# Kernel optimization log

Measured on AMD Instinct MI355X. Metric: run time of the kernel, lower is better.

## Reference

```python
import jax, jax.numpy as jnp
import numpy as np
import math

B, L, T, NW, D, DL = 4, 48, 16, 20, 256, 64


def setup_inputs() -> dict:
    key = jax.random.key(0)
    ks = jax.random.split(key, 16)
    n = lambda k, s, sc=1.0: jax.random.normal(k, s, dtype=jnp.float32) * sc
    z = lambda s: jnp.zeros(s, dtype=jnp.float32)
    return {
        'f_c': n(ks[0], (B, L, L, T, D), 0.5),
        'f_m': n(ks[1], (B, L, L, D), 0.5),
        'f_b': n(ks[2], (B, L, D), 0.5),
        'f_w': n(ks[3], (B, NW, D), 0.5),
        'f_s': n(ks[4], (B, D), 0.5),
        'bWq': n(ks[5], (D, D), 0.02), 'bbq': z((D,)),
        'bWk': n(ks[6], (D, D), 0.02), 'bbk': z((D,)),
        'cWq': n(ks[7], (DL, DL), 0.05), 'cbq': z((DL,)),
        'cWk': n(ks[8], (DL, DL), 0.05), 'cbk': z((DL,)),
        'dcc_w': n(ks[9], (DL, D), 0.05), 'dcc_b': z((DL,)),
        'dcw_w': n(ks[10], (DL, D), 0.05), 'dcw_b': z((DL,)),
        'dcs_w': n(ks[11], (DL, D), 0.05), 'dcs_b': z((DL,)),
        'ucc_w': n(ks[12], (D, DL), 0.05), 'ucc_b': z((D,)),
        'mfb_w': n(ks[13], (L, L), 0.05), 'mfb_b': z((L,)),
        'mfc_w': n(ks[14], (L, L), 0.05), 'mfc_b': z((L,)),
    }


def _smi_forward(f_c, f_m, f_b, f_w, f_s, bWq, bbq, bWk, bbk, cWq, cbq, cWk, cbk,
                 dcc_w, dcc_b, dcw_w, dcw_b, dcs_w, dcs_b, ucc_w, ucc_b,
                 mfb_w, mfb_b, mfc_w, mfc_b):
    lin = lambda x, W, b: x @ W.T + b  # torch Linear / 1x1 conv over channel-last

    def boundary_unit(fb, fm):
        # cross attention over words
        q = lin(fb, bWq, bbq)                                   # (B,L,D)
        k = lin(f_w, bWk, bbk)                                  # (B,Nw,D)
        aw = jax.nn.softmax(jnp.einsum('bld,bnd->bln', q, k) / math.sqrt(D), axis=-1)
        f_baq = jnp.einsum('bln,bnd->bld', aw, f_w)
        f_bq = fb * (f_baq + f_s[:, None, :])
        A_b = jax.nn.softmax(jnp.einsum('bld,bmd->blm', f_bq, f_bq) / math.sqrt(D), axis=-1)
        f_bb = jnp.einsum('blm,bmd->bld', A_b, fb)
        g_m = jax.nn.sigmoid(fm * f_s[:, None, None, :])        # (B,L,L,D)
        f_bm = jnp.einsum('blm,blmd->bld', A_b, g_m * fm)
        return f_bb + fb + f_bm

    def content_unit(fc, fm):
        f_c_hat = lin(fc, dcc_w, dcc_b)                         # (B,L,L,T,dl)
        f_w_hat = lin(f_w, dcw_w, dcw_b)                        # (B,Nw,dl)
        f_s_hat = lin(f_s, dcs_w, dcs_b)                        # (B,dl)
        q = lin(f_c_hat, cWq, cbq)
        k = lin(f_w_hat, cWk, cbk)
        aw = jax.nn.softmax(jnp.einsum('blmtd,bnd->blmtn', q, k) / math.sqrt(DL), axis=-1)
        f_caq = jnp.einsum('blmtn,bnd->blmtd', aw, f_w_hat)
        f_cq = f_c_hat * (f_caq + f_s_hat[:, None, None, None, :])
        A_c = jax.nn.softmax(jnp.einsum('blmtd,blmsd->blmts', f_cq, f_cq) / math.sqrt(DL), axis=-1)
        f_cc_hat = jnp.einsum('blmts,blmsd->blmtd', A_c, f_c_hat)
        f_cc = lin(f_cc_hat, ucc_w, ucc_b)                      # (B,L,L,T,D)
        g_m = jax.nn.sigmoid(fm * f_s[:, None, None, :])
        return f_cc + fc + (g_m * fm)[:, :, :, None, :]

    def moment_unit(fc, fm, fb):
        prod = fb[:, :, None, :] * fb[:, None, :, :]            # (B,L,L,D)
        conv_fb = jnp.einsum('oi,bimd->bomd', mfb_w, prod) + mfb_b[None, :, None, None]
        fc_mean = jnp.mean(fc, axis=3)                          # (B,L,L,D)
        conv_fc = jnp.einsum('oi,bimd->bomd', mfc_w, fc_mean) + mfc_b[None, :, None, None]
        return conv_fb + conv_fc + fm

    cu, bu, mu = f_c, f_b, f_m
    for _ in range(3):
        cu_n = content_unit(cu, mu)
        bu_n = boundary_unit(bu, mu)
        mu = moment_unit(cu_n, mu, bu_n)
        cu, bu = cu_n, bu_n
    return (mu, bu)


def reference(f_c, f_m, f_b, f_w, f_s, bWq, bbq, bWk, bbk, cWq, cbq, cWk, cbk,
              dcc_w, dcc_b, dcw_w, dcw_b, dcs_w, dcs_b, ucc_w, ucc_b,
              mfb_w, mfb_b, mfc_w, mfc_b):
    return _smi_forward(f_c, f_m, f_b, f_w, f_s, bWq, bbq, bWk, bbk, cWq, cbq, cWk, cbk,
                        dcc_w, dcc_b, dcw_w, dcw_b, dcs_w, dcs_b, ucc_w, ucc_b,
                        mfb_w, mfb_b, mfc_w, mfc_b)
```

## Files before the change

### kernel.cpp

```cpp
#include <hip/hip_runtime.h>

#define BB 4
#define LL 48
#define TT 16
#define NWW 20
#define DD 256
#define DLL 64

typedef __attribute__((ext_vector_type(8))) short s8v;
typedef __attribute__((ext_vector_type(4))) float f4v;
typedef unsigned short ushort_t;

#define OFF_CU     0ull
#define OFF_CM     75497472ull
#define OFF_BU0    84934656ull
#define OFF_BU1    85131264ull
#define OFF_FBQ    85327872ull
#define OFF_FWH    85524480ull
#define OFF_FSH    85544960ull
#define OFF_KB     85545984ull
#define OFF_BWQT   85627904ull
#define OFF_WBT    85890048ull
#define OFF_WCT    85899264ull
#define OFF_DCCF   85908480ull
#define OFF_CWQF   85941248ull
#define OFF_UCCF   85949440ull
#define OFF_KCF    85982208ull
#define OFF_FWHTF  85998592ull

static __device__ __forceinline__ ushort_t f2bf(float f){
  unsigned u = __float_as_uint(f);
  return (ushort_t)((u + 0x7FFFu + ((u>>16)&1u)) >> 16);
}
static __device__ __forceinline__ float bf2f(ushort_t h){
  return __uint_as_float(((unsigned)h)<<16);
}
static __device__ __forceinline__ void st64(void* p, float a, float b, float c, float d){
  uint2 v; v.x = (unsigned)f2bf(a) | ((unsigned)f2bf(b)<<16);
  v.y = (unsigned)f2bf(c) | ((unsigned)f2bf(d)<<16);
  *(uint2*)p = v;
}

#define ADR64(row, cb) (((row)<<7) + ((cb) ^ (((row)&7)<<4)))
#define ADR32(row, cb) (((row)<<6) + ((cb) ^ (((row)&3)<<4)))

#define MFMA(a,b,c) __builtin_amdgcn_mfma_f32_16x16x32_bf16((a),(b),(c),0,0,0)

template<int FIRST>
__global__ __launch_bounds__(256)
void content_kernel(const void* cusrc_, ushort_t* cudst, float* __restrict__ cm,
                    const float* __restrict__ fm_src, const float* __restrict__ fsg,
                    const float* __restrict__ fsh, const float* __restrict__ dccb,
                    const float* __restrict__ cbq, const float* __restrict__ uccb,
                    const ushort_t* __restrict__ dccf, const ushort_t* __restrict__ cwqf,
                    const ushort_t* __restrict__ uccf, const ushort_t* __restrict__ kcf,
                    const ushort_t* __restrict__ fwhtf)
{
  __shared__ __align__(16) char sm_all[4][8192];
  const int wid = threadIdx.x >> 6;
  const int lane = threadIdx.x & 63;
  char* sm = sm_all[wid];
  const int t = lane & 15, g = lane >> 4;
  const int tile = blockIdx.x*4 + wid;
  const int b = tile / (LL*LL);

  {
    f4v z = {0.f,0.f,0.f,0.f};
    *(f4v*)(sm + 4096 + ADR32(lane, 32)) = z;
    *(f4v*)(sm + 4096 + ADR32(lane, 48)) = z;
  }

  s8v xb[8];
  if (FIRST){
    const float* xp = (const float*)cusrc_ + (size_t)tile*4096 + t*DD + g*8;
    #pragma unroll
    for (int kk=0;kk<8;kk++){
      f4v lo = *(const f4v*)(xp + kk*32);
      f4v hi = *(const f4v*)(xp + kk*32 + 4);
      s8v v;
      v[0]=(short)f2bf(lo[0]); v[1]=(short)f2bf(lo[1]);
      v[2]=(short)f2bf(lo[2]); v[3]=(short)f2bf(lo[3]);
      v[4]=(short)f2bf(hi[0]); v[5]=(short)f2bf(hi[1]);
      v[6]=(short)f2bf(hi[2]); v[7]=(short)f2bf(hi[3]);
      xb[kk]=v;
    }
  } else {
    const ushort_t* xp = (const ushort_t*)cusrc_ + (size_t)tile*4096 + t*DD + g*8;
    #pragma unroll
    for (int kk=0;kk<8;kk++) xb[kk] = *(const s8v*)(xp + kk*32);
  }

  f4v accH[4];
  {
    f4v z = {0.f,0.f,0.f,0.f};
    accH[0]=z; accH[1]=z; accH[2]=z; accH[3]=z;
  }
  #pragma unroll
  for (int kk=0;kk<8;kk++){
    #pragma unroll
    for (int m0=0;m0<4;m0++){
      s8v a = *(const s8v*)(dccf + (((m0<<3)+kk)<<9) + (lane<<3));
      accH[m0] = MFMA(a, xb[kk], accH[m0]);
    }
  }
  #pragma unroll
  for (int m0=0;m0<4;m0++){
    f4v acc = accH[m0];
    f4v bi = *(const f4v*)(dccb + m0*16 + g*4);
    acc[0]+=bi[0]; acc[1]+=bi[1]; acc[2]+=bi[2]; acc[3]+=bi[3];
    accH[m0]=acc;
    st64(sm + ADR64(t, m0*32 + g*8), acc[0],acc[1],acc[2],acc[3]);
    #pragma unroll
    for (int r=0;r<4;r++)
      *(ushort_t*)(sm + 4096 + ADR32(m0*16 + g*4 + r, t*2)) = f2bf(acc[r]);
  }
  __syncthreads();

  s8v hb0 = *(const s8v*)(sm + ADR64(t, g*16));
  s8v hb1 = *(const s8v*)(sm + ADR64(t, 64 + g*16));
  #pragma unroll
  for (int m0=0;m0<4;m0++){
    f4v acc = {0.f,0.f,0.f,0.f};
    s8v a0 = *(const s8v*)(cwqf + (((m0<<1)  )<<9) + (lane<<3));
    s8v a1 = *(const s8v*)(cwqf + (((m0<<1)+1)<<9) + (lane<<3));
    acc = MFMA(a0, hb0, acc);
    acc = MFMA(a1, hb1, acc);
    f4v bi = *(const f4v*)(cbq + m0*16 + g*4);
    st64(sm + 2048 + ADR64(t, m0*32 + g*8),
         acc[0]+bi[0], acc[1]+bi[1], acc[2]+bi[2], acc[3]+bi[3]);
  }
  __syncthreads();

  s8v qb0 = *(const s8v*)(sm + 2048 + ADR64(t, g*16));
  s8v qb1 = *(const s8v*)(sm + 2048 + ADR64(t, 64 + g*16));
  f4v sA[2];
  #pragma unroll
  for (int m0=0;m0<2;m0++){
    f4v acc = {0.f,0.f,0.f,0.f};
    s8v a0 = *(const s8v*)(kcf + (b<<11) + (((m0<<1)  )<<9) + (lane<<3));
    s8v a1 = *(const s8v*)(kcf + (b<<11) + (((m0<<1)+1)<<9) + (lane<<3));
    acc = MFMA(a0, qb0, acc);
    acc = MFMA(a1, qb1, acc);
    sA[m0]=acc;
  }
  float mx = -3.0e38f;
  #pragma unroll
  for (int m0=0;m0<2;m0++){
    #pragma unroll
    for (int r=0;r<4;r++){
      int n = m0*16 + g*4 + r;
      if (n < NWW) mx = fmaxf(mx, sA[m0][r]);
    }
  }
  mx = fmaxf(mx, __shfl_xor(mx, 16));
  mx = fmaxf(mx, __shfl_xor(mx, 32));
  float ex[8]; float sum = 0.f;
  #pragma unroll
  for (int m0=0;m0<2;m0++){
    #pragma unroll
    for (int r=0;r<4;r++){
      int n = m0*16 + g*4 + r;
      float e = (n < NWW) ? __expf(sA[m0][r]-mx) : 0.f;
      ex[m0*4+r]=e; sum+=e;
    }
  }
  sum += __shfl_xor(sum,16);
  sum += __shfl_xor(sum,32);
  float inv = 1.f/sum;
  #pragma unroll
  for (int m0=0;m0<2;m0++)
    st64(sm + ADR32(t, m0*32 + g*8),
         ex[m0*4]*inv, ex[m0*4+1]*inv, ex[m0*4+2]*inv, ex[m0*4+3]*inv);
  __syncthreads();

  s8v awb = *(const s8v*)(sm + ADR32(t, g*16));
  __syncthreads();
  #pragma unroll
  for (int m0=0;m0<4;m0++){
    s8v a = *(const s8v*)(fwhtf + (b<<11) + (m0<<9) + (lane<<3));
    f4v z = {0.f,0.f,0.f,0.f};
    f4v acc = MFMA(a, awb, z);
    f4v fv = *(const f4v*)(fsh + b*DLL + m0*16 + g*4);
    float cq0 = accH[m0][0]*(acc[0]+fv[0])*0.35355339059f;
    float cq1 = accH[m0][1]*(acc[1]+fv[1])*0.35355339059f;
    float cq2 = accH[m0][2]*(acc[2]+fv[2])*0.35355339059f;
    float cq3 = accH[m0][3]*(acc[3]+fv[3])*0.35355339059f;
    ushort_t h0=f2bf(cq0),h1=f2bf(cq1),h2=f2bf(cq2),h3=f2bf(cq3);
    uint2 hv; hv.x=(unsigned)h0|((unsigned)h1<<16); hv.y=(unsigned)h2|((unsigned)h3<<16);
    *(uint2*)(sm + 2048 + ADR64(t, m0*32+g*8)) = hv;
    uint2 lv;
    lv.x = (unsigned)f2bf(cq0-bf2f(h0)) | ((unsigned)f2bf(cq1-bf2f(h1))<<16);
    lv.y = (unsigned)f2bf(cq2-bf2f(h2)) | ((unsigned)f2bf(cq3-bf2f(h3))<<16);
    *(uint2*)(sm + ADR64(t, m0*32+g*8)) = lv;
  }
  __syncthreads();

  s8v ch0 = *(const s8v*)(sm + 2048 + ADR64(t, g*16));
  s8v ch1 = *(const s8v*)(sm + 2048 + ADR64(t, 64+g*16));
  s8v cl0 = *(const s8v*)(sm + ADR64(t, g*16));
  s8v cl1 = *(const s8v*)(sm + ADR64(t, 64+g*16));
  f4v s2 = {0.f,0.f,0.f,0.f};
  s2 = MFMA(ch0, ch0, s2); s2 = MFMA(ch1, ch1, s2);
  s2 = MFMA(ch0, cl0, s2); s2 = MFMA(ch1, cl1, s2);
  s2 = MFMA(cl0, ch0, s2); s2 = MFMA(cl1, ch1, s2);
  float mx2 = fmaxf(fmaxf(s2[0],s2[1]), fmaxf(s2[2],s2[3]));
  mx2 = fmaxf(mx2, __shfl_xor(mx2,16));
  mx2 = fmaxf(mx2, __shfl_xor(mx2,32));
  float e0=__expf(s2[0]-mx2), e1=__expf(s2[1]-mx2), e2=__expf(s2[2]-mx2), e3=__expf(s2[3]-mx2);
  float su = e0+e1+e2+e3;
  su += __shfl_xor(su,16);
  su += __shfl_xor(su,32);
  float inv2 = 1.f/su;
  __syncthreads();
  st64(sm + ADR32(t, g*8), e0*inv2, e1*inv2, e2*inv2, e3*inv2);
  { uint2 zz; zz.x=0u; zz.y=0u; *(uint2*)(sm + ADR32(t, 32+g*8)) = zz; }
  __syncthreads();

  s8v acb = *(const s8v*)(sm + ADR32(t, g*16));
  #pragma unroll
  for (int m0=0;m0<4;m0++){
    s8v a = *(const s8v*)(sm + 4096 + ADR32(m0*16 + t, g*16));
    f4v z = {0.f,0.f,0.f,0.f};
    f4v acc = MFMA(a, acb, z);
    st64(sm + 2048 + ADR64(t, m0*32+g*8), acc[0],acc[1],acc[2],acc[3]);
  }
  __syncthreads();

  s8v cc0 = *(const s8v*)(sm + 2048 + ADR64(t, g*16));
  s8v cc1 = *(const s8v*)(sm + 2048 + ADR64(t, 64+g*16));
  __syncthreads();
  const float* fmp = fm_src + (size_t)tile*DD;
  const float* fsp = fsg + b*DD;
  ushort_t* op = cudst + (size_t)tile*4096 + t*DD;
  const float* xf = (const float*)cusrc_ + (size_t)tile*4096 + t*DD;
  const ushort_t* xh = (const ushort_t*)cusrc_ + (size_t)tile*4096 + t*DD;
  #pragma unroll
  for (int m0=0;m0<16;m0++){
    f4v acc = {0.f,0.f,0.f,0.f};
    s8v a0 = *(const s8v*)(uccf + (((m0<<1)  )<<9) + (lane<<3));
    s8v a1 = *(const s8v*)(uccf + (((m0<<1)+1)<<9) + (lane<<3));
    acc = MFMA(a0, cc0, acc);
    acc = MFMA(a1, cc1, acc);
    const int dq = m0*16 + g*4;
    f4v ub  = *(const f4v*)(uccb + dq);
    f4v fmv = *(const f4v*)(fmp + dq);
    f4v fvv = *(const f4v*)(fsp + dq);
    float xr0,xr1,xr2,xr3;
    if (FIRST){
      f4v xv = *(const f4v*)(xf + dq);
      xr0=xv[0]; xr1=xv[1]; xr2=xv[2]; xr3=xv[3];
    } else {
      uint2 xv = *(const uint2*)(xh + dq);
      xr0=bf2f((ushort_t)(xv.x&0xffffu)); xr1=bf2f((ushort_t)(xv.x>>16));
      xr2=bf2f((ushort_t)(xv.y&0xffffu)); xr3=bf2f((ushort_t)(xv.y>>16));
    }
    float o0 = acc[0]+ub[0]+xr0 + fmv[0]/(1.f+__expf(-fmv[0]*fvv[0]));
    float o1 = acc[1]+ub[1]+xr1 + fmv[1]/(1.f+__expf(-fmv[1]*fvv[1]));
    float o2 = acc[2]+ub[2]+xr2 + fmv[2]/(1.f+__expf(-fmv[2]*fvv[2]));
    float o3 = acc[3]+ub[3]+xr3 + fmv[3]/(1.f+__expf(-fmv[3]*fvv[3]));
    uint2 ov; ov.x=(unsigned)f2bf(o0)|((unsigned)f2bf(o1)<<16);
    ov.y=(unsigned)f2bf(o2)|((unsigned)f2bf(o3)<<16);
    *(uint2*)(op + dq) = ov;
    *(uint2*)(sm + (t<<9) + ((dq*2) ^ ((t&15)<<3))) = ov;
  }
  __syncthreads();

  {
    const int d0 = lane*4;
    float s0=0.f,s1=0.f,s2=0.f,s3=0.f;
    #pragma unroll
    for (int tt=0;tt<TT;tt++){
      uint2 v = *(const uint2*)(sm + (tt<<9) + ((d0*2) ^ ((tt&15)<<3)));
      s0 += bf2f((ushort_t)(v.x&0xffffu)); s1 += bf2f((ushort_t)(v.x>>16));
      s2 += bf2f((ushort_t)(v.y&0xffffu)); s3 += bf2f((ushort_t)(v.y>>16));
    }
    f4v o = {s0*0.0625f, s1*0.0625f, s2*0.0625f, s3*0.0625f};
    *(f4v*)(cm + (size_t)tile*DD + d0) = o;
  }
}

__global__ __launch_bounds__(256)
void bnd1_kernel(const float* __restrict__ fb, const float* __restrict__ f_w,
                 const float* __restrict__ f_s, const float* __restrict__ kb,
                 const float* __restrict__ bWqT, const float* __restrict__ bbq,
                 float* __restrict__ fbq)
{
  int blk = blockIdx.x; int b = blk / LL, l = blk % LL;
  int d = threadIdx.x;
  __shared__ float fbrow[DD];
  __shared__ float qrow[DD];
  __shared__ float smx[32];
  fbrow[d] = fb[(size_t)(b*LL+l)*DD + d];
  __syncthreads();
  float q = bbq[d];
  for (int e=0;e<DD;e++) q += fbrow[e]*bWqT[(size_t)e*DD+d];
  qrow[d]=q;
  __syncthreads();
  if (d < NWW){
    float s=0.f; const float* kr = kb + (size_t)(b*NWW+d)*DD;
    for (int e=0;e<DD;e++) s += qrow[e]*kr[e];
    smx[d] = s*(1.0f/16.0f);
  }
  __syncthreads();
  if (d==0){
    float m2=-3.0e38f;
    for(int n=0;n<NWW;n++) m2=fmaxf(m2,smx[n]);
    float su=0.f;
    for(int n=0;n<NWW;n++){ float e=__expf(smx[n]-m2); smx[n]=e; su+=e; }
    float iv=1.f/su;
    for(int n=0;n<NWW;n++) smx[n]*=iv;
  }
  __syncthreads();
  float acc=0.f;
  for (int n=0;n<NWW;n++) acc += smx[n]*f_w[(size_t)(b*NWW+n)*DD+d];
  fbq[(size_t)(b*LL+l)*DD+d] = fbrow[d]*(acc + f_s[b*DD+d]);
}

__global__ __launch_bounds__(256)
void bnd2_kernel(const float* __restrict__ fbq, const float* __restrict__ fb,
                 const float* __restrict__ fm, const float* __restrict__ f_s,
                 float* __restrict__ bu_out)
{
  int blk = blockIdx.x; int b = blk/LL, l = blk%LL;
  int d = threadIdx.x;
  __shared__ float Sl[DD];
  __shared__ float aw[LL];
  Sl[d] = fbq[(size_t)(b*LL+l)*DD + d];
  __syncthreads();
  if (d < LL){
    float s=0.f; const float* fr = fbq + (size_t)(b*LL+d)*DD;
    const f4v* s4 = (const f4v*)Sl; const f4v* f4p = (const f4v*)fr;
    for (int e=0;e<DD/4;e++){
      f4v a=s4[e], c=f4p[e];
      s += a[0]*c[0]+a[1]*c[1]+a[2]*c[2]+a[3]*c[3];
    }
    aw[d] = s*(1.0f/16.0f);
  }
  __syncthreads();
  if (d==0){
    float m2=-3.0e38f;
    for(int n=0;n<LL;n++) m2=fmaxf(m2,aw[n]);
    float su=0.f;
    for(int n=0;n<LL;n++){ float e=__expf(aw[n]-m2); aw[n]=e; su+=e; }
    float iv=1.f/su;
    for(int n=0;n<LL;n++) aw[n]*=iv;
  }
  __syncthreads();
  float fsd = f_s[b*DD+d];
  const float* fmrow = fm + ((size_t)(b*LL+l)*LL)*DD + d;
  float acc=0.f;
  for (int m=0;m<LL;m++){
    float a  = aw[m];
    float fbv= fb[(size_t)(b*LL+m)*DD+d];
    float fmv= fmrow[(size_t)m*DD];
    float gm = 1.f/(1.f+__expf(-fmv*fsd));
    acc += a*(fbv + gm*fmv);
  }
  bu_out[(size_t)(b*LL+l)*DD+d] = acc + fb[(size_t)(b*LL+l)*DD+d];
}

__global__ __launch_bounds__(256)
void moment_kernel(const float* __restrict__ cm, const float* __restrict__ bu,
                   const float* __restrict__ mu_in, float* __restrict__ mu_out,
                   const float* __restrict__ wbT, const float* __restrict__ wcT,
                   const float* __restrict__ mfbb, const float* __restrict__ mfcb)
{
  int blk = blockIdx.x;
  int oh = blk & 1; int bm = blk>>1; int b = bm/LL, m = bm%LL;
  int d = threadIdx.x;
  const int ob = oh*24;
  float accB[24], accC[24];
  #pragma unroll
  for (int o=0;o<24;o++){accB[o]=0.f;accC[o]=0.f;}
  for (int i=0;i<LL;i++){
    float bv = bu[(size_t)(b*LL+i)*DD+d];
    float cv = cm[((size_t)(b*LL+i)*LL+m)*DD+d];
    const float* wb = wbT + i*LL + ob;
    const float* wc = wcT + i*LL + ob;
    #pragma unroll
    for (int o=0;o<24;o+=4){
      f4v w1 = *(const f4v*)(wb+o);
      f4v w2 = *(const f4v*)(wc+o);
      accB[o  ]+=w1[0]*bv; accB[o+1]+=w1[1]*bv; accB[o+2]+=w1[2]*bv; accB[o+3]+=w1[3]*bv;
      accC[o  ]+=w2[0]*cv; accC[o+1]+=w2[1]*cv; accC[o+2]+=w2[2]*cv; accC[o+3]+=w2[3]*cv;
    }
  }
  float bum = bu[(size_t)(b*LL+m)*DD+d];
  #pragma unroll
  for (int o=0;o<24;o++){
    int oo = ob+o;
    size_t oi = ((size_t)(b*LL+oo)*LL+m)*DD + d;
    mu_out[oi] = accB[o]*bum + mfbb[oo] + accC[o] + mfcb[oo] + mu_in[oi];
  }
}

__global__ __launch_bounds__(256)
void prep1_kernel(const float* __restrict__ f_w, const float* __restrict__ f_s,
                  const float* __restrict__ bWq, const float* __restrict__ bWk,
                  const float* __restrict__ bbk,
                  const float* __restrict__ dcw_w, const float* __restrict__ dcw_b,
                  const float* __restrict__ dcs_w, const float* __restrict__ dcs_b,
                  const float* __restrict__ dcc_w, const float* __restrict__ cWq,
                  const float* __restrict__ ucc_w,
                  const float* __restrict__ mfb_w, const float* __restrict__ mfc_w,
                  float* __restrict__ kb, float* __restrict__ fwh,
                  float* __restrict__ fsh, float* __restrict__ bWqT,
                  ushort_t* __restrict__ dccf, ushort_t* __restrict__ cwqf,
                  ushort_t* __restrict__ uccf,
                  float* __restrict__ wbT, float* __restrict__ wcT)
{
  const int S0=20480, S1=5120, S2=256, S3=65536, S4=16384, S5=4096, S6=16384, S7=2304;
  const int TOT = S0+S1+S2+S3+S4+S5+S6+S7;
  int id = blockIdx.x*256 + threadIdx.x;
  int nth = gridDim.x*256;
  for (int x=id; x<TOT; x+=nth){
    int y=x;
    if (y < S0){
      int b=y/(NWW*DD); int r=y%(NWW*DD); int n=r/DD, dd2=r%DD;
      float s=bbk[dd2];
      const float* fr=f_w+(size_t)(b*NWW+n)*DD; const float* wr=bWk+(size_t)dd2*DD;
      for(int e=0;e<DD;e++) s+=fr[e]*wr[e];
      kb[y]=s; continue; }
    y-=S0;
    if (y < S1){
      int b=y/(NWW*DLL); int r=y%(NWW*DLL); int n=r/DLL, dl=r%DLL;
      float s=dcw_b[dl];
      const float* fr=f_w+(size_t)(b*NWW+n)*DD; const float* wr=dcw_w+(size_t)dl*DD;
      for(int e=0;e<DD;e++) s+=fr[e]*wr[e];
      fwh[y]=s; continue; }
    y-=S1;
    if (y < S2){
      int b=y/DLL, dl=y%DLL;
      float s=dcs_b[dl];
      const float* fr=f_s+(size_t)b*DD; const float* wr=dcs_w+(size_t)dl*DD;
      for(int e=0;e<DD;e++) s+=fr[e]*wr[e];
      fsh[y]=s; continue; }
    y-=S2;
    if (y < S3){ int e=y/DD, dd2=y%DD; bWqT[y] = bWq[(size_t)dd2*DD+e]; continue; }
    y-=S3;
    if (y < S4){
      int j=y&7, ln=(y>>3)&63, kk=(y>>9)&7, m0=y>>12;
      int mm=m0*16+(ln&15), k=kk*32+((ln>>4)<<3)+j;
      dccf[y]=f2bf(dcc_w[(size_t)mm*DD+k]); continue; }
    y-=S4;
    if (y < S5){
      int j=y&7, ln=(y>>3)&63, kk=(y>>9)&1, m0=y>>10;
      int mm=m0*16+(ln&15), k=kk*32+((ln>>4)<<3)+j;
      cwqf[y]=f2bf(cWq[(size_t)mm*DLL+k]); continue; }
    y-=S5;
    if (y < S6){
      int j=y&7, ln=(y>>3)&63, kk=(y>>9)&1, m0=y>>10;
      int mm=m0*16+(ln&15), k=kk*32+((ln>>4)<<3)+j;
      uccf[y]=f2bf(ucc_w[(size_t)mm*DLL+k]); continue; }
    y-=S6;
    { int i=y/LL, o=y%LL; wbT[y]=mfb_w[(size_t)o*LL+i]; wcT[y]=mfc_w[(size_t)o*LL+i]; }
  }
}

__global__ __launch_bounds__(256)
void prep2_kernel(const float* __restrict__ fwh, const float* __restrict__ cWk,
                  const float* __restrict__ cbk,
                  ushort_t* __restrict__ kcf, ushort_t* __restrict__ fwhtf)
{
  const int S0 = BB*2048, S1 = BB*2048;
  int id = blockIdx.x*256+threadIdx.x; int nth=gridDim.x*256;
  for (int x=id; x<S0+S1; x+=nth){
    int y=x;
    if (y < S0){
      int b=y>>11; int z=y&2047;
      int j=z&7, ln=(z>>3)&63, kk=(z>>9)&1, m0=z>>10;
      int n=m0*16+(ln&15), k=kk*32+((ln>>4)<<3)+j;
      float v=0.f;
      if (n<NWW){
        float s=cbk[k];
        const float* fr=fwh+(size_t)(b*NWW+n)*DLL; const float* wr=cWk+(size_t)k*DLL;
        for(int e=0;e<DLL;e++) s+=fr[e]*wr[e];
        v=s*0.125f;
      }
      kcf[y]=f2bf(v); continue; }
    y-=S0;
    {
      int b=y>>11; int z=y&2047;
      int j=z&7, ln=(z>>3)&63, m0=z>>9;
      int dl=m0*16+(ln&15), n=((ln>>4)<<3)+j;
      float v = (n<NWW)? fwh[(size_t)(b*NWW+n)*DLL+dl] : 0.f;
      fwhtf[y]=f2bf(v);
    }
  }
}

extern "C" void kernel_launch(void* const* d_in, const int* in_sizes, int n_in,
                              void* d_out, int out_size, void* d_ws, size_t ws_size,
                              hipStream_t stream)
{
  (void)in_sizes; (void)n_in; (void)out_size; (void)ws_size;
  const float* f_c  = (const float*)d_in[0];
  const float* f_m  = (const float*)d_in[1];
  const float* f_b  = (const float*)d_in[2];
  const float* f_w  = (const float*)d_in[3];
  const float* f_s  = (const float*)d_in[4];
  const float* bWq  = (const float*)d_in[5];
  const float* bbq  = (const float*)d_in[6];
  const float* bWk  = (const float*)d_in[7];
  const float* bbk  = (const float*)d_in[8];
  const float* cWq  = (const float*)d_in[9];
  const float* cbq  = (const float*)d_in[10];
  const float* cWk  = (const float*)d_in[11];
  const float* cbk  = (const float*)d_in[12];
  const float* dcc_w= (const float*)d_in[13];
  const float* dcc_b= (const float*)d_in[14];
  const float* dcw_w= (const float*)d_in[15];
  const float* dcw_b= (const float*)d_in[16];
  const float* dcs_w= (const float*)d_in[17];
  const float* dcs_b= (const float*)d_in[18];
  const float* ucc_w= (const float*)d_in[19];
  const float* ucc_b= (const float*)d_in[20];
  const float* mfb_w= (const float*)d_in[21];
  const float* mfb_b= (const float*)d_in[22];
  const float* mfc_w= (const float*)d_in[23];
  const float* mfc_b= (const float*)d_in[24];

  char* ws = (char*)d_ws;
  ushort_t* cu = (ushort_t*)(ws+OFF_CU);
  float* cmr  = (float*)(ws+OFF_CM);
  float* bu0  = (float*)(ws+OFF_BU0);
  float* bu1  = (float*)(ws+OFF_BU1);
  float* fbq  = (float*)(ws+OFF_FBQ);
  float* fwh  = (float*)(ws+OFF_FWH);
  float* fsh  = (float*)(ws+OFF_FSH);
  float* kb   = (float*)(ws+OFF_KB);
  float* bWqT = (float*)(ws+OFF_BWQT);
  float* wbT  = (float*)(ws+OFF_WBT);
  float* wcT  = (float*)(ws+OFF_WCT);
  ushort_t* dccf = (ushort_t*)(ws+OFF_DCCF);
  ushort_t* cwqf = (ushort_t*)(ws+OFF_CWQF);
  ushort_t* uccf = (ushort_t*)(ws+OFF_UCCF);
  ushort_t* kcf  = (ushort_t*)(ws+OFF_KCF);
  ushort_t* fwhtf= (ushort_t*)(ws+OFF_FWHTF);

  float* mu = (float*)d_out;
  float* out_bu = (float*)d_out + 2359296;

  prep1_kernel<<<128,256,0,stream>>>(f_w,f_s,bWq,bWk,bbk,dcw_w,dcw_b,dcs_w,dcs_b,
                                     dcc_w,cWq,ucc_w,mfb_w,mfc_w,
                                     kb,fwh,fsh,bWqT,dccf,cwqf,uccf,wbT,wcT);
  prep2_kernel<<<32,256,0,stream>>>(fwh,cWk,cbk,kcf,fwhtf);

  float* bu_cur = nullptr;
  for (int it=0; it<3; ++it){
    const float* fmsrc = (it==0)? f_m : mu;
    if (it==0)
      content_kernel<1><<<2304,256,0,stream>>>(f_c, cu, cmr, fmsrc, f_s, fsh, dcc_b, cbq, ucc_b,
                                               dccf,cwqf,uccf,kcf,fwhtf);
    else
      content_kernel<0><<<2304,256,0,stream>>>(cu, cu, cmr, fmsrc, f_s, fsh, dcc_b, cbq, ucc_b,
                                               dccf,cwqf,uccf,kcf,fwhtf);
    const float* fbsrc = (it==0)? f_b : bu_cur;
    float* bunew = (it==2)? out_bu : ((it==0)? bu0 : ((bu_cur==bu0)? bu1 : bu0));
    bnd1_kernel<<<192,256,0,stream>>>(fbsrc, f_w, f_s, kb, bWqT, bbq, fbq);
    bnd2_kernel<<<192,256,0,stream>>>(fbq, fbsrc, fmsrc, f_s, bunew);
    moment_kernel<<<384,256,0,stream>>>(cmr, bunew, fmsrc, mu, wbT, wcT, mfb_b, mfc_b);
    bu_cur = bunew;
  }
}
```

Before: 425.4 us.

## Split each content tile across two waves instead of one wave per tile

The content kernel previously gave each 64-lane wave its own (b,l,m) tile and ran four independent tiles per 256-thread block. Now each tile is handled by a 128-thread block of two waves, each computing half of the output channels in the projection GEMMs. The small softmax stages run on wave 0 only, and the per-tile mean is split over both waves. This halves per-wave register use and serial MFMA chains to raise parallelism, at the cost of extra block barriers, an idle wave during the softmax stages, and redundant input loads in both waves.

```diff
diff --git a/kernel.cpp b/kernel.cpp
--- a/kernel.cpp
+++ b/kernel.cpp
@@ -47,7 +47,7 @@
 #define MFMA(a,b,c) __builtin_amdgcn_mfma_f32_16x16x32_bf16((a),(b),(c),0,0,0)
 
 template<int FIRST>
-__global__ __launch_bounds__(256)
+__global__ __launch_bounds__(128)
 void content_kernel(const void* cusrc_, ushort_t* cudst, float* __restrict__ cm,
                     const float* __restrict__ fm_src, const float* __restrict__ fsg,
                     const float* __restrict__ fsh, const float* __restrict__ dccb,
@@ -56,18 +56,16 @@
                     const ushort_t* __restrict__ uccf, const ushort_t* __restrict__ kcf,
                     const ushort_t* __restrict__ fwhtf)
 {
-  __shared__ __align__(16) char sm_all[4][8192];
-  const int wid = threadIdx.x >> 6;
+  __shared__ __align__(16) char sm[8192];
+  const int w = threadIdx.x >> 6;
   const int lane = threadIdx.x & 63;
-  char* sm = sm_all[wid];
   const int t = lane & 15, g = lane >> 4;
-  const int tile = blockIdx.x*4 + wid;
+  const int tile = blockIdx.x;
   const int b = tile / (LL*LL);
 
   {
     f4v z = {0.f,0.f,0.f,0.f};
-    *(f4v*)(sm + 4096 + ADR32(lane, 32)) = z;
-    *(f4v*)(sm + 4096 + ADR32(lane, 48)) = z;
+    *(f4v*)(sm + 4096 + ADR32(lane, 32 + w*16)) = z;
   }
 
   s8v xb[8];
@@ -90,25 +88,19 @@
     for (int kk=0;kk<8;kk++) xb[kk] = *(const s8v*)(xp + kk*32);
   }
 
-  f4v accH[4];
-  {
-    f4v z = {0.f,0.f,0.f,0.f};
-    accH[0]=z; accH[1]=z; accH[2]=z; accH[3]=z;
-  }
-  #pragma unroll
-  for (int kk=0;kk<8;kk++){
-    #pragma unroll
-    for (int m0=0;m0<4;m0++){
+  f4v accH[2];
+  #pragma unroll
+  for (int i=0;i<2;i++){
+    const int m0 = 2*w + i;
+    f4v acc = {0.f,0.f,0.f,0.f};
+    #pragma unroll
+    for (int kk=0;kk<8;kk++){
       s8v a = *(const s8v*)(dccf + (((m0<<3)+kk)<<9) + (lane<<3));
-      accH[m0] = MFMA(a, xb[kk], accH[m0]);
-    }
-  }
-  #pragma unroll
-  for (int m0=0;m0<4;m0++){
-    f4v acc = accH[m0];
+      acc = MFMA(a, xb[kk], acc);
+    }
     f4v bi = *(const f4v*)(dccb + m0*16 + g*4);
     acc[0]+=bi[0]; acc[1]+=bi[1]; acc[2]+=bi[2]; acc[3]+=bi[3];
-    accH[m0]=acc;
+    accH[i]=acc;
     st64(sm + ADR64(t, m0*32 + g*8), acc[0],acc[1],acc[2],acc[3]);
     #pragma unroll
     for (int r=0;r<4;r++)
@@ -119,7 +111,8 @@
   s8v hb0 = *(const s8v*)(sm + ADR64(t, g*16));
   s8v hb1 = *(const s8v*)(sm + ADR64(t, 64 + g*16));
   #pragma unroll
-  for (int m0=0;m0<4;m0++){
+  for (int i=0;i<2;i++){
+    const int m0 = 2*w + i;
     f4v acc = {0.f,0.f,0.f,0.f};
     s8v a0 = *(const s8v*)(cwqf + (((m0<<1)  )<<9) + (lane<<3));
     s8v a1 = *(const s8v*)(cwqf + (((m0<<1)+1)<<9) + (lane<<3));
@@ -131,60 +124,63 @@
   }
   __syncthreads();
 
-  s8v qb0 = *(const s8v*)(sm + 2048 + ADR64(t, g*16));
-  s8v qb1 = *(const s8v*)(sm + 2048 + ADR64(t, 64 + g*16));
-  f4v sA[2];
-  #pragma unroll
-  for (int m0=0;m0<2;m0++){
-    f4v acc = {0.f,0.f,0.f,0.f};
-    s8v a0 = *(const s8v*)(kcf + (b<<11) + (((m0<<1)  )<<9) + (lane<<3));
-    s8v a1 = *(const s8v*)(kcf + (b<<11) + (((m0<<1)+1)<<9) + (lane<<3));
-    acc = MFMA(a0, qb0, acc);
-    acc = MFMA(a1, qb1, acc);
-    sA[m0]=acc;
-  }
-  float mx = -3.0e38f;
-  #pragma unroll
-  for (int m0=0;m0<2;m0++){
-    #pragma unroll
-    for (int r=0;r<4;r++){
-      int n = m0*16 + g*4 + r;
-      if (n < NWW) mx = fmaxf(mx, sA[m0][r]);
-    }
-  }
-  mx = fmaxf(mx, __shfl_xor(mx, 16));
-  mx = fmaxf(mx, __shfl_xor(mx, 32));
-  float ex[8]; float sum = 0.f;
-  #pragma unroll
-  for (int m0=0;m0<2;m0++){
-    #pragma unroll
-    for (int r=0;r<4;r++){
-      int n = m0*16 + g*4 + r;
-      float e = (n < NWW) ? __expf(sA[m0][r]-mx) : 0.f;
-      ex[m0*4+r]=e; sum+=e;
-    }
-  }
-  sum += __shfl_xor(sum,16);
-  sum += __shfl_xor(sum,32);
-  float inv = 1.f/sum;
-  #pragma unroll
-  for (int m0=0;m0<2;m0++)
-    st64(sm + ADR32(t, m0*32 + g*8),
-         ex[m0*4]*inv, ex[m0*4+1]*inv, ex[m0*4+2]*inv, ex[m0*4+3]*inv);
+  if (w==0){
+    s8v qb0 = *(const s8v*)(sm + 2048 + ADR64(t, g*16));
+    s8v qb1 = *(const s8v*)(sm + 2048 + ADR64(t, 64 + g*16));
+    f4v sA[2];
+    #pragma unroll
+    for (int m0=0;m0<2;m0++){
+      f4v acc = {0.f,0.f,0.f,0.f};
+      s8v a0 = *(const s8v*)(kcf + (b<<11) + (((m0<<1)  )<<9) + (lane<<3));
+      s8v a1 = *(const s8v*)(kcf + (b<<11) + (((m0<<1)+1)<<9) + (lane<<3));
+      acc = MFMA(a0, qb0, acc);
+      acc = MFMA(a1, qb1, acc);
+      sA[m0]=acc;
+    }
+    float mx = -3.0e38f;
+    #pragma unroll
+    for (int m0=0;m0<2;m0++){
+      #pragma unroll
+      for (int r=0;r<4;r++){
+        int n = m0*16 + g*4 + r;
+        if (n < NWW) mx = fmaxf(mx, sA[m0][r]);
+      }
+    }
+    mx = fmaxf(mx, __shfl_xor(mx, 16));
+    mx = fmaxf(mx, __shfl_xor(mx, 32));
+    float ex[8]; float sum = 0.f;
+    #pragma unroll
+    for (int m0=0;m0<2;m0++){
+      #pragma unroll
+      for (int r=0;r<4;r++){
+        int n = m0*16 + g*4 + r;
+        float e = (n < NWW) ? __expf(sA[m0][r]-mx) : 0.f;
+        ex[m0*4+r]=e; sum+=e;
+      }
+    }
+    sum += __shfl_xor(sum,16);
+    sum += __shfl_xor(sum,32);
+    float inv = 1.f/sum;
+    #pragma unroll
+    for (int m0=0;m0<2;m0++)
+      st64(sm + ADR32(t, m0*32 + g*8),
+           ex[m0*4]*inv, ex[m0*4+1]*inv, ex[m0*4+2]*inv, ex[m0*4+3]*inv);
+  }
   __syncthreads();
 
   s8v awb = *(const s8v*)(sm + ADR32(t, g*16));
   __syncthreads();
   #pragma unroll
-  for (int m0=0;m0<4;m0++){
+  for (int i=0;i<2;i++){
+    const int m0 = 2*w + i;
     s8v a = *(const s8v*)(fwhtf + (b<<11) + (m0<<9) + (lane<<3));
     f4v z = {0.f,0.f,0.f,0.f};
     f4v acc = MFMA(a, awb, z);
     f4v fv = *(const f4v*)(fsh + b*DLL + m0*16 + g*4);
-    float cq0 = accH[m0][0]*(acc[0]+fv[0])*0.35355339059f;
-    float cq1 = accH[m0][1]*(acc[1]+fv[1])*0.35355339059f;
-    float cq2 = accH[m0][2]*(acc[2]+fv[2])*0.35355339059f;
-    float cq3 = accH[m0][3]*(acc[3]+fv[3])*0.35355339059f;
+    float cq0 = accH[i][0]*(acc[0]+fv[0])*0.35355339059f;
+    float cq1 = accH[i][1]*(acc[1]+fv[1])*0.35355339059f;
+    float cq2 = accH[i][2]*(acc[2]+fv[2])*0.35355339059f;
+    float cq3 = accH[i][3]*(acc[3]+fv[3])*0.35355339059f;
     ushort_t h0=f2bf(cq0),h1=f2bf(cq1),h2=f2bf(cq2),h3=f2bf(cq3);
     uint2 hv; hv.x=(unsigned)h0|((unsigned)h1<<16); hv.y=(unsigned)h2|((unsigned)h3<<16);
     *(uint2*)(sm + 2048 + ADR64(t, m0*32+g*8)) = hv;
@@ -195,30 +191,35 @@
   }
   __syncthreads();
 
-  s8v ch0 = *(const s8v*)(sm + 2048 + ADR64(t, g*16));
-  s8v ch1 = *(const s8v*)(sm + 2048 + ADR64(t, 64+g*16));
-  s8v cl0 = *(const s8v*)(sm + ADR64(t, g*16));
-  s8v cl1 = *(const s8v*)(sm + ADR64(t, 64+g*16));
-  f4v s2 = {0.f,0.f,0.f,0.f};
-  s2 = MFMA(ch0, ch0, s2); s2 = MFMA(ch1, ch1, s2);
-  s2 = MFMA(ch0, cl0, s2); s2 = MFMA(ch1, cl1, s2);
-  s2 = MFMA(cl0, ch0, s2); s2 = MFMA(cl1, ch1, s2);
-  float mx2 = fmaxf(fmaxf(s2[0],s2[1]), fmaxf(s2[2],s2[3]));
-  mx2 = fmaxf(mx2, __shfl_xor(mx2,16));
-  mx2 = fmaxf(mx2, __shfl_xor(mx2,32));
-  float e0=__expf(s2[0]-mx2), e1=__expf(s2[1]-mx2), e2=__expf(s2[2]-mx2), e3=__expf(s2[3]-mx2);
-  float su = e0+e1+e2+e3;
-  su += __shfl_xor(su,16);
-  su += __shfl_xor(su,32);
-  float inv2 = 1.f/su;
-  __syncthreads();
-  st64(sm + ADR32(t, g*8), e0*inv2, e1*inv2, e2*inv2, e3*inv2);
-  { uint2 zz; zz.x=0u; zz.y=0u; *(uint2*)(sm + ADR32(t, 32+g*8)) = zz; }
+  if (w==0){
+    s8v ch0 = *(const s8v*)(sm + 2048 + ADR64(t, g*16));
+    s8v ch1 = *(const s8v*)(sm + 2048 + ADR64(t, 64+g*16));
+    s8v cl0 = *(const s8v*)(sm + ADR64(t, g*16));
+    s8v cl1 = *(const s8v*)(sm + ADR64(t, 64+g*16));
+    f4v s2 = {0.f,0.f,0.f,0.f};
+    s2 = MFMA(ch0, ch0, s2); s2 = MFMA(ch1, ch1, s2);
+    s2 = MFMA(ch0, cl0, s2); s2 = MFMA(ch1, cl1, s2);
+    s2 = MFMA(cl0, ch0, s2); s2 = MFMA(cl1, ch1, s2);
+    float mx2 = fmaxf(fmaxf(s2[0],s2[1]), fmaxf(s2[2],s2[3]));
+    mx2 = fmaxf(mx2, __shfl_xor(mx2,16));
+    mx2 = fmaxf(mx2, __shfl_xor(mx2,32));
+    float e0=__expf(s2[0]-mx2), e1=__expf(s2[1]-mx2), e2=__expf(s2[2]-mx2), e3=__expf(s2[3]-mx2);
+    float su = e0+e1+e2+e3;
+    su += __shfl_xor(su,16);
+    su += __shfl_xor(su,32);
+    float inv2 = 1.f/su;
+    __syncthreads();
+    st64(sm + ADR32(t, g*8), e0*inv2, e1*inv2, e2*inv2, e3*inv2);
+    { uint2 zz; zz.x=0u; zz.y=0u; *(uint2*)(sm + ADR32(t, 32+g*8)) = zz; }
+  } else {
+    __syncthreads();
+  }
   __syncthreads();
 
   s8v acb = *(const s8v*)(sm + ADR32(t, g*16));
   #pragma unroll
-  for (int m0=0;m0<4;m0++){
+  for (int i=0;i<2;i++){
+    const int m0 = 2*w + i;
     s8v a = *(const s8v*)(sm + 4096 + ADR32(m0*16 + t, g*16));
     f4v z = {0.f,0.f,0.f,0.f};
     f4v acc = MFMA(a, acb, z);
@@ -235,7 +236,8 @@
   const float* xf = (const float*)cusrc_ + (size_t)tile*4096 + t*DD;
   const ushort_t* xh = (const ushort_t*)cusrc_ + (size_t)tile*4096 + t*DD;
   #pragma unroll
-  for (int m0=0;m0<16;m0++){
+  for (int i=0;i<8;i++){
+    const int m0 = w*8 + i;
     f4v acc = {0.f,0.f,0.f,0.f};
     s8v a0 = *(const s8v*)(uccf + (((m0<<1)  )<<9) + (lane<<3));
     s8v a1 = *(const s8v*)(uccf + (((m0<<1)+1)<<9) + (lane<<3));
@@ -266,16 +268,15 @@
   __syncthreads();
 
   {
-    const int d0 = lane*4;
-    float s0=0.f,s1=0.f,s2=0.f,s3=0.f;
+    const int d0 = threadIdx.x*2;
+    float s0=0.f,s1=0.f;
     #pragma unroll
     for (int tt=0;tt<TT;tt++){
-      uint2 v = *(const uint2*)(sm + (tt<<9) + ((d0*2) ^ ((tt&15)<<3)));
-      s0 += bf2f((ushort_t)(v.x&0xffffu)); s1 += bf2f((ushort_t)(v.x>>16));
-      s2 += bf2f((ushort_t)(v.y&0xffffu)); s3 += bf2f((ushort_t)(v.y>>16));
-    }
-    f4v o = {s0*0.0625f, s1*0.0625f, s2*0.0625f, s3*0.0625f};
-    *(f4v*)(cm + (size_t)tile*DD + d0) = o;
+      unsigned v = *(const unsigned*)(sm + (tt<<9) + ((d0*2) ^ ((tt&15)<<3)));
+      s0 += bf2f((ushort_t)(v&0xffffu)); s1 += bf2f((ushort_t)(v>>16));
+    }
+    float2 o = {s0*0.0625f, s1*0.0625f};
+    *(float2*)(cm + (size_t)tile*DD + d0) = o;
   }
 }
 
@@ -550,10 +551,10 @@
   for (int it=0; it<3; ++it){
     const float* fmsrc = (it==0)? f_m : mu;
     if (it==0)
-      content_kernel<1><<<2304,256,0,stream>>>(f_c, cu, cmr, fmsrc, f_s, fsh, dcc_b, cbq, ucc_b,
+      content_kernel<1><<<9216,128,0,stream>>>(f_c, cu, cmr, fmsrc, f_s, fsh, dcc_b, cbq, ucc_b,
                                                dccf,cwqf,uccf,kcf,fwhtf);
     else
-      content_kernel<0><<<2304,256,0,stream>>>(cu, cu, cmr, fmsrc, f_s, fsh, dcc_b, cbq, ucc_b,
+      content_kernel<0><<<9216,128,0,stream>>>(cu, cu, cmr, fmsrc, f_s, fsh, dcc_b, cbq, ucc_b,
                                                dccf,cwqf,uccf,kcf,fwhtf);
     const float* fbsrc = (it==0)? f_b : bu_cur;
     float* bunew = (it==2)? out_bu : ((it==0)? bu0 : ((bu_cur==bu0)? bu1 : bu0));
```

After: 462.7 us. 1.09x slower.
